# Optimization experiments

Measured on AMD Instinct MI355X. Metric: run time of the kernel, lower is better.

Reference implementation:

```python
import jax, jax.numpy as jnp
import numpy as np

N_CLASSES = 80
SEG_LEN = 512          # boxes per class (uniform segments)
H = 128                # hidden_size
DH = 2 * H             # decoder hidden (= concat of bidirectional encoder final hiddens)
EMB = 32               # decoder_input_dim
SOS, EOS = 2, 3


def _gru_cell(x, h, Wih, Whh, bih, bhh):
    # PyTorch GRU cell math. x:(in,), h:(hid,), Wih:(3*hid,in), Whh:(3*hid,hid)
    gi = Wih @ x + bih
    gh = Whh @ h + bhh
    i_r, i_z, i_n = jnp.split(gi, 3)
    h_r, h_z, h_n = jnp.split(gh, 3)
    r = jax.nn.sigmoid(i_r + h_r)
    z = jax.nn.sigmoid(i_z + h_z)
    n = jnp.tanh(i_n + r * h_n)
    return (1.0 - z) * n + z * h


def _gru_seq(xs, h0, Wih, Whh, bih, bhh):
    # xs: (T, in); returns final hidden (hid,) and all hiddens (T, hid)
    def step(h, x):
        h2 = _gru_cell(x, h, Wih, Whh, bih, bhh)
        return h2, h2
    hT, hs = jax.lax.scan(step, h0, xs)
    return hT, hs

# vmap over the 80 classes (per-class weights)
_run_gru = jax.vmap(_gru_seq, in_axes=(0, 0, 0, 0, 0, 0))


def setup_inputs() -> dict:
    key = jax.random.key(0)
    ks = jax.random.split(key, 32)
    N = N_CLASSES * SEG_LEN
    s = 0.05
    inp = {
        "feat": jax.random.normal(ks[0], (N, 1024), jnp.float32),
        "score": jax.random.uniform(ks[1], (N, 1), jnp.float32),
        "box": jax.random.uniform(ks[2], (N, 4), jnp.float32),
        "origin_score": jax.random.uniform(ks[3], (N, 91), jnp.float32),
        "labels": jax.random.randint(ks[4], (N,), 0, 2, jnp.int64),
        "weights": jax.random.uniform(ks[5], (N,), jnp.float32),
        "unique_class": jnp.ones((N_CLASSES,), jnp.int64),
        "unique_class_len": jnp.arange(N_CLASSES + 1, dtype=jnp.int64) * SEG_LEN,
        # shared linears
        "appear_W": jax.random.normal(ks[6], (H, 1024), jnp.float32) * s,
        "appear_b": jnp.zeros((H,), jnp.float32),
        "featlin_W": jax.random.normal(ks[7], (H, H + 96), jnp.float32) * s,
        "featlin_b": jnp.zeros((H,), jnp.float32),
        # per-class bidirectional encoder GRUs
        "enc_Wih_f": jax.random.normal(ks[8], (N_CLASSES, 3 * H, H), jnp.float32) * s,
        "enc_Whh_f": jax.random.normal(ks[9], (N_CLASSES, 3 * H, H), jnp.float32) * s,
        "enc_bih_f": jnp.zeros((N_CLASSES, 3 * H), jnp.float32),
        "enc_bhh_f": jnp.zeros((N_CLASSES, 3 * H), jnp.float32),
        "enc_Wih_b": jax.random.normal(ks[10], (N_CLASSES, 3 * H, H), jnp.float32) * s,
        "enc_Whh_b": jax.random.normal(ks[11], (N_CLASSES, 3 * H, H), jnp.float32) * s,
        "enc_bih_b": jnp.zeros((N_CLASSES, 3 * H), jnp.float32),
        "enc_bhh_b": jnp.zeros((N_CLASSES, 3 * H), jnp.float32),
        # decoder
        "dec_emb": jax.random.normal(ks[12], (4, EMB), jnp.float32) * s,
        "dec_Wih": jax.random.normal(ks[13], (N_CLASSES, 3 * DH, EMB), jnp.float32) * s,
        "dec_Whh": jax.random.normal(ks[14], (N_CLASSES, 3 * DH, DH), jnp.float32) * s,
        "dec_bih": jnp.zeros((N_CLASSES, 3 * DH), jnp.float32),
        "dec_bhh": jnp.zeros((N_CLASSES, 3 * DH), jnp.float32),
        "out_W": jax.random.normal(ks[15], (4, DH), jnp.float32) * s,
        "out_b": jnp.zeros((4,), jnp.float32),
    }
    return inp


def reference(feat, score, box, origin_score, labels, weights, unique_class,
              unique_class_len, appear_W, appear_b, featlin_W, featlin_b,
              enc_Wih_f, enc_Whh_f, enc_bih_f, enc_bhh_f,
              enc_Wih_b, enc_Whh_b, enc_bih_b, enc_bhh_b,
              dec_emb, dec_Wih, dec_Whh, dec_bih, dec_bhh, out_W, out_b):
    # --- shared feature encoding ---
    x = jax.nn.relu(feat @ appear_W.T + appear_b)                    # (N, H)
    allf = jnp.concatenate([x, score, box, origin_score], axis=1)    # (N, H+96)
    enc_feat = jax.nn.relu(allf @ featlin_W.T + featlin_b)           # (N, H)

    # --- per-class bidirectional encoder (uniform segments) ---
    seg = enc_feat.reshape(N_CLASSES, SEG_LEN, H)
    eos = jnp.ones((N_CLASSES, 1, H), enc_feat.dtype)                # encoder_EOS = ones
    enc_in = jnp.concatenate([seg, eos], axis=1)                     # (80, L+1, H)
    h0 = jnp.zeros((N_CLASSES, H), enc_feat.dtype)
    h_f, _ = _run_gru(enc_in, h0, enc_Wih_f, enc_Whh_f, enc_bih_f, enc_bhh_f)
    h_b, _ = _run_gru(enc_in[:, ::-1], h0, enc_Wih_b, enc_Whh_b, enc_bih_b, enc_bhh_b)
    dec_h0 = jnp.concatenate([h_f, h_b], axis=-1)                    # (80, 2H)

    # --- per-class decoder with teacher forcing (SOS then gold labels) ---
    emb = dec_emb[labels].reshape(N_CLASSES, SEG_LEN, EMB)
    sos = jnp.broadcast_to(dec_emb[SOS], (N_CLASSES, 1, EMB))
    dec_in = jnp.concatenate([sos, emb], axis=1)                     # (80, L+1, EMB)
    _, dec_hs = _run_gru(dec_in, dec_h0, dec_Wih, dec_Whh, dec_bih, dec_bhh)

    logits = dec_hs.reshape(-1, DH) @ out_W.T + out_b                # (80*(L+1), 4)
    output = jax.nn.log_softmax(logits, axis=-1)
    return output, labels, weights
```

## Files before the change

kernel.cpp:

```cpp
#include <hip/hip_runtime.h>


typedef __fp16 h2v __attribute__((ext_vector_type(2)));
typedef __fp16 h8 __attribute__((ext_vector_type(8)));

__device__ __forceinline__ h2v pk2(float a, float b) {
  return __builtin_amdgcn_cvt_pkrtz(a, b);
}
__device__ __forceinline__ unsigned h2u(h2v h) { return __builtin_bit_cast(unsigned, h); }
__device__ __forceinline__ h2v u2h(unsigned u) { return __builtin_bit_cast(h2v, u); }
__device__ __forceinline__ float fdot2f(h2v a, h2v b, float c) {
  return __builtin_amdgcn_fdot2(a, b, c, false);
}
__device__ __forceinline__ float sigf(float x) { return 1.f / (1.f + __expf(-x)); }
__device__ __forceinline__ float tanhfast(float x) { return 2.f / (1.f + __expf(-2.f * x)) - 1.f; }

__device__ __forceinline__ h8 pack8(float4 a, float4 b) {
  h2v p0 = pk2(a.x, a.y), p1 = pk2(a.z, a.w), p2 = pk2(b.x, b.y), p3 = pk2(b.z, b.w);
  return (h8){p0[0], p0[1], p1[0], p1[1], p2[0], p2[1], p3[0], p3[1]};
}

#define SL(V, j) (__builtin_shufflevector((V), (V), 2 * (j), 2 * (j) + 1))

template <int CTRL>
__device__ __forceinline__ float dppadd(float acc, float v) {
  int r = __builtin_amdgcn_update_dpp(0, __float_as_int(v), CTRL, 0xF, 0xF, true);
  return acc + __int_as_float(r);
}
__device__ __forceinline__ float swz4add(float acc, float v) {
  return acc + __int_as_float(__builtin_amdgcn_ds_swizzle(__float_as_int(v), 0x101F));
}

__device__ __forceinline__ float reduce8s(float p0, float p1, float p2, float p3,
                                          float p4, float p5, float p6, float p7) {
  p0 = dppadd<0xB1>(p0, p1);
  p2 = dppadd<0xB1>(p2, p3);
  p4 = dppadd<0xB1>(p4, p5);
  p6 = dppadd<0xB1>(p6, p7);
  p0 = dppadd<0x4E>(p0, p2);
  p4 = dppadd<0x4E>(p4, p6);
  p0 = swz4add(p0, p4);
  p0 = dppadd<0x128>(p0, p0);
  return p0;
}

__device__ __forceinline__ float dot4(h8 V, h2v a0, h2v a1, h2v a2, h2v a3, float acc) {
  acc = fdot2f(SL(V, 0), a0, acc);
  acc = fdot2f(SL(V, 1), a1, acc);
  acc = fdot2f(SL(V, 2), a2, acc);
  acc = fdot2f(SL(V, 3), a3, acc);
  return acc;
}

__global__ void k_fill_misc(const float* __restrict__ score, const float* __restrict__ box,
                            const float* __restrict__ orig, float* __restrict__ allf) {
  int i = blockIdx.x * blockDim.x + threadIdx.x;
  if (i >= 40960 * 96) return;
  int row = i / 96, k = i - row * 96;
  float v;
  if (k == 0) v = score[row];
  else if (k < 5) v = box[row * 4 + (k - 1)];
  else v = orig[(size_t)row * 91 + (k - 5)];
  allf[(size_t)row * 224 + 128 + k] = v;
}

__global__ __launch_bounds__(256) void k_gemm_appear(
    const float* __restrict__ A, const float* __restrict__ W,
    const float* __restrict__ bias, float* __restrict__ allf) {
  __shared__ float As[32][68];
  __shared__ float Ws[32][132];
  const int tid = threadIdx.x;
  const int tx = tid & 15, ty = tid >> 4;
  const int r0 = blockIdx.x * 64;
  const int lr = tid >> 3;
  const int lk = (tid & 7) * 4;
  float acc[4][8];
#pragma unroll
  for (int i = 0; i < 4; ++i)
#pragma unroll
    for (int j = 0; j < 8; ++j) acc[i][j] = 0.f;

  for (int k0 = 0; k0 < 1024; k0 += 32) {
#pragma unroll
    for (int i = 0; i < 2; ++i) {
      int rr = lr + i * 32;
      float4 v = *(const float4*)(A + (size_t)(r0 + rr) * 1024 + k0 + lk);
      As[lk + 0][rr] = v.x; As[lk + 1][rr] = v.y; As[lk + 2][rr] = v.z; As[lk + 3][rr] = v.w;
    }
#pragma unroll
    for (int i = 0; i < 4; ++i) {
      int wr = lr + i * 32;
      float4 v = *(const float4*)(W + (size_t)wr * 1024 + k0 + lk);
      Ws[lk + 0][wr] = v.x; Ws[lk + 1][wr] = v.y; Ws[lk + 2][wr] = v.z; Ws[lk + 3][wr] = v.w;
    }
    __syncthreads();
#pragma unroll
    for (int kk = 0; kk < 32; ++kk) {
      float4 a = *(const float4*)&As[kk][ty * 4];
      float4 w0 = *(const float4*)&Ws[kk][tx * 8];
      float4 w1 = *(const float4*)&Ws[kk][tx * 8 + 4];
      float av[4] = {a.x, a.y, a.z, a.w};
      float wv[8] = {w0.x, w0.y, w0.z, w0.w, w1.x, w1.y, w1.z, w1.w};
#pragma unroll
      for (int i = 0; i < 4; ++i)
#pragma unroll
        for (int j = 0; j < 8; ++j) acc[i][j] = fmaf(av[i], wv[j], acc[i][j]);
    }
    __syncthreads();
  }
#pragma unroll
  for (int i = 0; i < 4; ++i) {
    int row = r0 + ty * 4 + i;
#pragma unroll
    for (int j = 0; j < 8; ++j) {
      int col = tx * 8 + j;
      float v = acc[i][j] + bias[col];
      allf[(size_t)row * 224 + col] = fmaxf(v, 0.f);
    }
  }
}

__global__ __launch_bounds__(256) void k_gemm_featlin(
    const float* __restrict__ A, const float* __restrict__ W,
    const float* __restrict__ bias, unsigned* __restrict__ encf2) {
  __shared__ float As[32][68];
  __shared__ float Ws[32][132];
  const int tid = threadIdx.x;
  const int tx = tid & 15, ty = tid >> 4;
  const int r0 = blockIdx.x * 64;
  const int lr = tid >> 3;
  const int lk = (tid & 7) * 4;
  float acc[4][8];
#pragma unroll
  for (int i = 0; i < 4; ++i)
#pragma unroll
    for (int j = 0; j < 8; ++j) acc[i][j] = 0.f;

  for (int k0 = 0; k0 < 224; k0 += 32) {
#pragma unroll
    for (int i = 0; i < 2; ++i) {
      int rr = lr + i * 32;
      float4 v = *(const float4*)(A + (size_t)(r0 + rr) * 224 + k0 + lk);
      As[lk + 0][rr] = v.x; As[lk + 1][rr] = v.y; As[lk + 2][rr] = v.z; As[lk + 3][rr] = v.w;
    }
#pragma unroll
    for (int i = 0; i < 4; ++i) {
      int wr = lr + i * 32;
      float4 v = *(const float4*)(W + (size_t)wr * 224 + k0 + lk);
      Ws[lk + 0][wr] = v.x; Ws[lk + 1][wr] = v.y; Ws[lk + 2][wr] = v.z; Ws[lk + 3][wr] = v.w;
    }
    __syncthreads();
#pragma unroll
    for (int kk = 0; kk < 32; ++kk) {
      float4 a = *(const float4*)&As[kk][ty * 4];
      float4 w0 = *(const float4*)&Ws[kk][tx * 8];
      float4 w1 = *(const float4*)&Ws[kk][tx * 8 + 4];
      float av[4] = {a.x, a.y, a.z, a.w};
      float wv[8] = {w0.x, w0.y, w0.z, w0.w, w1.x, w1.y, w1.z, w1.w};
#pragma unroll
      for (int i = 0; i < 4; ++i)
#pragma unroll
        for (int j = 0; j < 8; ++j) acc[i][j] = fmaf(av[i], wv[j], acc[i][j]);
    }
    __syncthreads();
  }
#pragma unroll
  for (int i = 0; i < 4; ++i) {
    int row = r0 + ty * 4 + i;
    unsigned* orow = encf2 + (size_t)row * 64;
#pragma unroll
    for (int p = 0; p < 4; ++p) {
      int col = tx * 8 + 2 * p;
      float a = fmaxf(acc[i][2 * p] + bias[col], 0.f);
      float b = fmaxf(acc[i][2 * p + 1] + bias[col + 1], 0.f);
      orow[tx * 4 + p] = h2u(pk2(a, b));
    }
  }
}

__global__ __launch_bounds__(256) void k_dec_gi(
    const float* __restrict__ Wih, const float* __restrict__ bih,
    const float* __restrict__ emb, float* __restrict__ gi) {
  __shared__ float e[4][32];
  const int c = blockIdx.x, tid = threadIdx.x;
  if (tid < 128) e[tid >> 5][tid & 31] = emb[tid];
  __syncthreads();
#pragma unroll
  for (int i = 0; i < 3; ++i) {
    int r = tid + i * 256;
    const float* w = Wih + ((size_t)c * 768 + r) * 32;
    float b = bih[(size_t)c * 768 + r];
    float a0 = b, a1 = b, a2 = b, a3 = b;
#pragma unroll
    for (int k = 0; k < 32; ++k) {
      float wv = w[k];
      a0 = fmaf(wv, e[0][k], a0);
      a1 = fmaf(wv, e[1][k], a1);
      a2 = fmaf(wv, e[2][k], a2);
      a3 = fmaf(wv, e[3][k], a3);
    }
    gi[((size_t)c * 4 + 0) * 768 + r] = a0;
    gi[((size_t)c * 4 + 1) * 768 + r] = a1;
    gi[((size_t)c * 4 + 2) * 768 + r] = a2;
    gi[((size_t)c * 4 + 3) * 768 + r] = a3;
  }
}

#define ENCROW(k)                                                                   \
  h8 ci_##k, ch_##k, sg_##k;                                                        \
  {                                                                                 \
    int vc = 32 * w + 8 * q + ((k) ^ mw);                                           \
    const float4* pi = (const float4*)(Wih + (size_t)vc * 128 + 8 * m);             \
    ci_##k = pack8(pi[0], pi[1]);                                                   \
    __builtin_amdgcn_sched_barrier(0);                                              \
    const float4* ph = (const float4*)(Whh + (size_t)vc * 128 + 8 * m);             \
    ch_##k = pack8(ph[0], ph[1]);                                                   \
    __builtin_amdgcn_sched_barrier(0);                                              \
    int s = (w < 4) ? vc : (vc - 128);                                              \
    const float* sb =                                                               \
        (w < 4) ? (Wih + (size_t)(256 + s) * 128) : (Whh + (size_t)(256 + s) * 128);\
    const float4* ps = (const float4*)(sb + 8 * m);                                 \
    sg_##k = pack8(ps[0], ps[1]);                                                   \
    __builtin_amdgcn_sched_barrier(0);                                              \
  }

#define EDOTC(k) dot4(ci_##k, x0, x1, x2, x3, dot4(ch_##k, g0, g1, g2, g3, 0.f))
#define EDOTS(k) dot4(sg_##k, s0, s1, s2, s3, 0.f)

__global__ __launch_bounds__(512)
__attribute__((amdgpu_waves_per_eu(2, 2))) void k_enc_gru(
    const unsigned* __restrict__ encf2,
    const float* __restrict__ WihF, const float* __restrict__ WhhF,
    const float* __restrict__ bihF, const float* __restrict__ bhhF,
    const float* __restrict__ WihB, const float* __restrict__ WhhB,
    const float* __restrict__ bihB, const float* __restrict__ bhhB,
    float* __restrict__ dec_h0) {
  const int blk = blockIdx.x;
  const int c = blk >> 1, dir = blk & 1;
  const int tid = threadIdx.x;
  const int w = tid >> 6, l = tid & 63, q = l >> 4, m = l & 15, mw = m & 7;

  const float* Wih = (dir ? WihB : WihF) + (size_t)c * 384 * 128;
  const float* Whh = (dir ? WhhB : WhhF) + (size_t)c * 384 * 128;
  const float* bih = (dir ? bihB : bihF) + (size_t)c * 384;
  const float* bhh = (dir ? bhhB : bhhF) + (size_t)c * 384;

  __shared__ __align__(16) unsigned x2s[2][64];
  __shared__ __align__(16) unsigned h2s[64];
  __shared__ float aBuf[512];

  ENCROW(0) ENCROW(1) ENCROW(2) ENCROW(3)
  ENCROW(4) ENCROW(5) ENCROW(6) ENCROW(7)

  float bown;
  int ownIdx;
  if (m < 8) {
    int vo = 32 * w + 8 * q + m;
    bown = bih[vo] + bhh[vo];
    ownIdx = vo;
  } else {
    int so = (w < 4) ? (32 * w + 8 * q + mw) : (32 * (w - 4) + 8 * q + mw);
    bown = (w < 4) ? bih[256 + so] : bhh[256 + so];
    ownIdx = (w < 4) ? (256 + so) : (384 + so);
  }

  if (tid < 64) h2s[tid] = 0u;
  if (tid >= 448) {
    int lane = tid - 448;
    x2s[0][lane] = (dir == 0) ? encf2[((size_t)c * 512 + 0) * 64 + lane] : 0x3C003C00u;
  }
  float hreg = 0.f;
  __syncthreads();

  for (int t = 0; t <= 512; ++t) {
    unsigned xpre = 0;
    if (tid >= 448 && t < 512) {
      int tn = t + 1, lane = tid - 448;
      int row = (dir == 0) ? ((tn < 512) ? tn : -1) : (512 - tn);
      xpre = (row < 0) ? 0x3C003C00u : encf2[((size_t)c * 512 + row) * 64 + lane];
    }
    uint4 xv = ((const uint4*)&x2s[t & 1][0])[m];
    uint4 hv = ((const uint4*)&h2s[0])[m];
    h2v x0 = u2h(xv.x), x1 = u2h(xv.y), x2 = u2h(xv.z), x3 = u2h(xv.w);
    h2v g0 = u2h(hv.x), g1 = u2h(hv.y), g2 = u2h(hv.z), g3 = u2h(hv.w);
    float pA = reduce8s(EDOTC(0), EDOTC(1), EDOTC(2), EDOTC(3),
                        EDOTC(4), EDOTC(5), EDOTC(6), EDOTC(7));
    h2v s0 = (w < 4) ? x0 : g0, s1 = (w < 4) ? x1 : g1;
    h2v s2 = (w < 4) ? x2 : g2, s3 = (w < 4) ? x3 : g3;
    float pB = reduce8s(EDOTS(0), EDOTS(1), EDOTS(2), EDOTS(3),
                        EDOTS(4), EDOTS(5), EDOTS(6), EDOTS(7));
    aBuf[ownIdx] = ((m < 8) ? pA : pB) + bown;
    __syncthreads();
    if (tid < 128) {
      float r = sigf(aBuf[tid]);
      float z = sigf(aBuf[128 + tid]);
      float nn = tanhfast(aBuf[256 + tid] + r * aBuf[384 + tid]);
      float hn = (1.f - z) * nn + z * hreg;
      hreg = hn;
      float other = __shfl_xor(hn, 1, 64);
      if ((tid & 1) == 0) h2s[tid >> 1] = h2u(pk2(hn, other));
    } else if (tid >= 448 && t < 512) {
      x2s[(t + 1) & 1][tid - 448] = xpre;
    }
    __syncthreads();
  }
  if (tid < 128) dec_h0[(size_t)c * 256 + dir * 128 + tid] = hreg;
}

#define DECROW(kc, k)                                                               \
  h8 wA##kc##_##k, wB##kc##_##k;                                                    \
  {                                                                                 \
    int row = 64 * w + 16 * q + 8 * (kc) + ((k) ^ mw);                              \
    const float4* src = (const float4*)(Whh + ((size_t)c * 768 + row) * 256 + 16 * m);\
    float4 v0 = src[0], v1 = src[1];                                                \
    wA##kc##_##k = pack8(v0, v1);                                                   \
    __builtin_amdgcn_sched_barrier(0);                                              \
    float4 v2 = src[2], v3 = src[3];                                                \
    wB##kc##_##k = pack8(v2, v3);                                                   \
    __builtin_amdgcn_sched_barrier(0);                                              \
  }

#define DDOT(kc, k)                                                        \
  (fdot2f(SL(wB##kc##_##k, 3), g7,                                         \
   fdot2f(SL(wB##kc##_##k, 2), g6,                                         \
   fdot2f(SL(wB##kc##_##k, 1), g5,                                         \
   fdot2f(SL(wB##kc##_##k, 0), g4,                                         \
   fdot2f(SL(wA##kc##_##k, 3), g3,                                         \
   fdot2f(SL(wA##kc##_##k, 2), g2,                                         \
   fdot2f(SL(wA##kc##_##k, 1), g1,                                         \
   fdot2f(SL(wA##kc##_##k, 0), g0, 0.f)))))))))

__global__ __launch_bounds__(768)
__attribute__((amdgpu_waves_per_eu(3, 3))) void k_dec_gru(
    const float* __restrict__ Whh, const float* __restrict__ bhh,
    const float* __restrict__ gi, const float* __restrict__ h0,
    const int* __restrict__ labels,
    const float* __restrict__ outW, const float* __restrict__ outB,
    float* __restrict__ out) {
  const int c = blockIdx.x, tid = threadIdx.x;
  const int w = tid >> 6, l = tid & 63, q = l >> 4, m = l & 15, mw = m & 7;

  __shared__ __align__(16) unsigned h2s[128];
  __shared__ float aBuf[768];
  __shared__ float gisf[2304];
  __shared__ float owsh[1024];
  __shared__ int labs[513];
  __shared__ float red[4][4];

  DECROW(0, 0) DECROW(0, 1) DECROW(0, 2) DECROW(0, 3)
  DECROW(0, 4) DECROW(0, 5) DECROW(0, 6) DECROW(0, 7)
  DECROW(1, 0) DECROW(1, 1) DECROW(1, 2) DECROW(1, 3)
  DECROW(1, 4) DECROW(1, 5) DECROW(1, 6) DECROW(1, 7)

  float bown = bhh[(size_t)c * 768 + 64 * w + l];

  for (int i = tid; i < 2304; i += 768) gisf[i] = gi[(size_t)c * 4 * 768 + i];
  for (int i = tid; i < 1024; i += 768) owsh[i] = outW[i];
  if (tid < 512) labs[tid + 1] = labels[(size_t)c * 512 + tid];
  if (tid == 512) labs[0] = 2;
  float b0 = outB[0], b1 = outB[1], b2 = outB[2], b3 = outB[3];
  float hreg = 0.f;
  if (tid < 256) {
    hreg = h0[(size_t)c * 256 + tid];
    float other = __shfl_xor(hreg, 1, 64);
    if ((tid & 1) == 0) h2s[tid >> 1] = h2u(pk2(hreg, other));
  }
  __syncthreads();

  for (int t = 0; t <= 512; ++t) {
    const uint4* hp = (const uint4*)(&h2s[0]);
    uint4 ha = hp[2 * m], hb = hp[2 * m + 1];
    h2v g0 = u2h(ha.x), g1 = u2h(ha.y), g2 = u2h(ha.z), g3 = u2h(ha.w);
    h2v g4 = u2h(hb.x), g5 = u2h(hb.y), g6 = u2h(hb.z), g7 = u2h(hb.w);
    float pc0 = reduce8s(DDOT(0, 0), DDOT(0, 1), DDOT(0, 2), DDOT(0, 3),
                         DDOT(0, 4), DDOT(0, 5), DDOT(0, 6), DDOT(0, 7));
    float pc1 = reduce8s(DDOT(1, 0), DDOT(1, 1), DDOT(1, 2), DDOT(1, 3),
                         DDOT(1, 4), DDOT(1, 5), DDOT(1, 6), DDOT(1, 7));
    aBuf[64 * w + l] = ((m < 8) ? pc0 : pc1) + bown;
    __syncthreads();
    if (tid < 256) {
      int sel = labs[t];
      const float* gsel = &gisf[sel * 768];
      float r = sigf(gsel[tid] + aBuf[tid]);
      float z = sigf(gsel[256 + tid] + aBuf[256 + tid]);
      float nn = tanhfast(gsel[512 + tid] + r * aBuf[512 + tid]);
      float hn = (1.f - z) * nn + z * hreg;
      hreg = hn;
      float other = __shfl_xor(hn, 1, 64);
      if ((tid & 1) == 0) h2s[tid >> 1] = h2u(pk2(hn, other));
      float p0 = owsh[tid] * hn, p1 = owsh[256 + tid] * hn;
      float p2 = owsh[512 + tid] * hn, p3 = owsh[768 + tid] * hn;
#pragma unroll
      for (int off = 32; off > 0; off >>= 1) {
        p0 += __shfl_xor(p0, off, 64);
        p1 += __shfl_xor(p1, off, 64);
        p2 += __shfl_xor(p2, off, 64);
        p3 += __shfl_xor(p3, off, 64);
      }
      if ((tid & 63) == 0) {
        int ww = tid >> 6;
        red[ww][0] = p0; red[ww][1] = p1; red[ww][2] = p2; red[ww][3] = p3;
      }
    }
    __syncthreads();
    if (tid == 0) {
      float l0 = red[0][0] + red[1][0] + red[2][0] + red[3][0] + b0;
      float l1 = red[0][1] + red[1][1] + red[2][1] + red[3][1] + b1;
      float l2 = red[0][2] + red[1][2] + red[2][2] + red[3][2] + b2;
      float l3 = red[0][3] + red[1][3] + red[2][3] + red[3][3] + b3;
      float mm = fmaxf(fmaxf(l0, l1), fmaxf(l2, l3));
      float s = __expf(l0 - mm) + __expf(l1 - mm) + __expf(l2 - mm) + __expf(l3 - mm);
      float lse = mm + __logf(s);
      float* o = out + ((size_t)c * 513 + t) * 4;
      o[0] = l0 - lse; o[1] = l1 - lse; o[2] = l2 - lse; o[3] = l3 - lse;
    }
  }
}

__global__ void k_passthrough(const int* __restrict__ labels,
                              const float* __restrict__ weights,
                              float* __restrict__ out) {
  int i = blockIdx.x * blockDim.x + threadIdx.x;
  if (i < 40960) {
    out[164160 + i] = (float)labels[i];
    out[164160 + 40960 + i] = weights[i];
  }
}

extern "C" void kernel_launch(void* const* d_in, const int* in_sizes, int n_in,
                              void* d_out, int out_size, void* d_ws, size_t ws_size,
                              hipStream_t stream) {
  (void)in_sizes; (void)n_in; (void)out_size; (void)ws_size;
  const float* feat = (const float*)d_in[0];
  const float* score = (const float*)d_in[1];
  const float* box = (const float*)d_in[2];
  const float* orig = (const float*)d_in[3];
  const int* labels = (const int*)d_in[4];
  const float* weights = (const float*)d_in[5];
  const float* appear_W = (const float*)d_in[8];
  const float* appear_b = (const float*)d_in[9];
  const float* featlin_W = (const float*)d_in[10];
  const float* featlin_b = (const float*)d_in[11];
  const float* eWihF = (const float*)d_in[12];
  const float* eWhhF = (const float*)d_in[13];
  const float* ebihF = (const float*)d_in[14];
  const float* ebhhF = (const float*)d_in[15];
  const float* eWihB = (const float*)d_in[16];
  const float* eWhhB = (const float*)d_in[17];
  const float* ebihB = (const float*)d_in[18];
  const float* ebhhB = (const float*)d_in[19];
  const float* dec_emb = (const float*)d_in[20];
  const float* dWih = (const float*)d_in[21];
  const float* dWhh = (const float*)d_in[22];
  const float* dbih = (const float*)d_in[23];
  const float* dbhh = (const float*)d_in[24];
  const float* outW = (const float*)d_in[25];
  const float* outB = (const float*)d_in[26];
  float* out = (float*)d_out;

  char* ws = (char*)d_ws;
  float* allf = (float*)ws;
  unsigned* encf2 = (unsigned*)(ws + (size_t)40960 * 224 * 4);
  float* dec_h0 = (float*)(ws + (size_t)40960 * 224 * 4 + (size_t)40960 * 64 * 4);
  float* dec_gi = dec_h0 + 80 * 256;

  k_fill_misc<<<15360, 256, 0, stream>>>(score, box, orig, allf);
  k_gemm_appear<<<640, 256, 0, stream>>>(feat, appear_W, appear_b, allf);
  k_gemm_featlin<<<640, 256, 0, stream>>>(allf, featlin_W, featlin_b, encf2);
  k_dec_gi<<<80, 256, 0, stream>>>(dWih, dbih, dec_emb, dec_gi);
  k_enc_gru<<<160, 512, 0, stream>>>(encf2, eWihF, eWhhF, ebihF, ebhhF,
                                     eWihB, eWhhB, ebihB, ebhhB, dec_h0);
  k_dec_gru<<<80, 768, 0, stream>>>(dWhh, dbhh, dec_gi, dec_h0, labels, outW, outB, out);
  k_passthrough<<<160, 256, 0, stream>>>(labels, weights, out);
}
```

Baseline: 1.653 ms.

## Restructure encoder/decoder GRU steps to one barrier per step, split output projection

Both recurrent kernels are reorganised so each thread computes a full hidden unit's gates, with partners combined via lane shuffles. This removes the shared-memory gate buffer and cuts each timestep to a single barrier using double-buffered hidden state. Decoder weights are pre-packed to fp16 in a separate kernel, split across registers, LDS and per-step global streaming, and the block shrinks to 512 threads. The output projection and log-softmax move out of the serial loop into a parallel kernel over stored fp16 hidden states, at the cost of extra launches and workspace traffic.

After: 1.595 ms. 3.5% less time.

```diff
diff --git a/kernel.cpp b/kernel.cpp
--- a/kernel.cpp
+++ b/kernel.cpp
@@ -2,7 +2,6 @@
 
 
 typedef __fp16 h2v __attribute__((ext_vector_type(2)));
-typedef __fp16 h8 __attribute__((ext_vector_type(8)));
 
 __device__ __forceinline__ h2v pk2(float a, float b) {
   return __builtin_amdgcn_cvt_pkrtz(a, b);
@@ -15,12 +14,21 @@
 __device__ __forceinline__ float sigf(float x) { return 1.f / (1.f + __expf(-x)); }
 __device__ __forceinline__ float tanhfast(float x) { return 2.f / (1.f + __expf(-2.f * x)) - 1.f; }
 
-__device__ __forceinline__ h8 pack8(float4 a, float4 b) {
-  h2v p0 = pk2(a.x, a.y), p1 = pk2(a.z, a.w), p2 = pk2(b.x, b.y), p3 = pk2(b.z, b.w);
-  return (h8){p0[0], p0[1], p1[0], p1[1], p2[0], p2[1], p3[0], p3[1]};
-}
-
-#define SL(V, j) (__builtin_shufflevector((V), (V), 2 * (j), 2 * (j) + 1))
+__device__ __forceinline__ uint4 pack8u(float4 a, float4 b) {
+  uint4 o;
+  o.x = h2u(pk2(a.x, a.y)); o.y = h2u(pk2(a.z, a.w));
+  o.z = h2u(pk2(b.x, b.y)); o.w = h2u(pk2(b.z, b.w));
+  return o;
+}
+
+__device__ __forceinline__ float dotu4(uint4 cv, h2v a0, h2v a1, h2v a2, h2v a3,
+                                       float acc) {
+  acc = fdot2f(u2h(cv.x), a0, acc);
+  acc = fdot2f(u2h(cv.y), a1, acc);
+  acc = fdot2f(u2h(cv.z), a2, acc);
+  acc = fdot2f(u2h(cv.w), a3, acc);
+  return acc;
+}
 
 template <int CTRL>
 __device__ __forceinline__ float dppadd(float acc, float v) {
@@ -44,13 +52,10 @@
   return p0;
 }
 
-__device__ __forceinline__ float dot4(h8 V, h2v a0, h2v a1, h2v a2, h2v a3, float acc) {
-  acc = fdot2f(SL(V, 0), a0, acc);
-  acc = fdot2f(SL(V, 1), a1, acc);
-  acc = fdot2f(SL(V, 2), a2, acc);
-  acc = fdot2f(SL(V, 3), a3, acc);
-  return acc;
-}
+#define BAR_LGKM()                                     \
+  asm volatile("s_waitcnt lgkmcnt(0)" ::: "memory");   \
+  __builtin_amdgcn_s_barrier();                        \
+  asm volatile("" ::: "memory");
 
 __global__ void k_fill_misc(const float* __restrict__ score, const float* __restrict__ box,
                             const float* __restrict__ orig, float* __restrict__ allf) {
@@ -206,29 +211,30 @@
   }
 }
 
-#define ENCROW(k)                                                                   \
-  h8 ci_##k, ch_##k, sg_##k;                                                        \
-  {                                                                                 \
-    int vc = 32 * w + 8 * q + ((k) ^ mw);                                           \
-    const float4* pi = (const float4*)(Wih + (size_t)vc * 128 + 8 * m);             \
-    ci_##k = pack8(pi[0], pi[1]);                                                   \
-    __builtin_amdgcn_sched_barrier(0);                                              \
-    const float4* ph = (const float4*)(Whh + (size_t)vc * 128 + 8 * m);             \
-    ch_##k = pack8(ph[0], ph[1]);                                                   \
-    __builtin_amdgcn_sched_barrier(0);                                              \
-    int s = (w < 4) ? vc : (vc - 128);                                              \
-    const float* sb =                                                               \
-        (w < 4) ? (Wih + (size_t)(256 + s) * 128) : (Whh + (size_t)(256 + s) * 128);\
-    const float4* ps = (const float4*)(sb + 8 * m);                                 \
-    sg_##k = pack8(ps[0], ps[1]);                                                   \
-    __builtin_amdgcn_sched_barrier(0);                                              \
-  }
-
-#define EDOTC(k) dot4(ci_##k, x0, x1, x2, x3, dot4(ch_##k, g0, g1, g2, g3, 0.f))
-#define EDOTS(k) dot4(sg_##k, s0, s1, s2, s3, 0.f)
-
-__global__ __launch_bounds__(512)
-__attribute__((amdgpu_waves_per_eu(2, 2))) void k_enc_gru(
+__global__ __launch_bounds__(512) void k_pack_dec(
+    const float* __restrict__ Whh, uint4* __restrict__ wpk) {
+  const int c = blockIdx.x / 48, ic = blockIdx.x % 48;
+  const int tid = threadIdx.x;
+  const int G = tid >> 4, m = tid & 15, mw = m & 7;
+  const int gt = ic >> 4, k = (ic & 15) >> 1, hf = ic & 1;
+  const int row = gt * 256 + 8 * G + (k ^ mw);
+  const float* src = Whh + ((size_t)c * 768 + row) * 256 + 16 * m + 8 * hf;
+  wpk[((size_t)c * 48 + ic) * 512 + tid] =
+      pack8u(*(const float4*)src, *(const float4*)(src + 4));
+}
+
+#define ELOAD(gt, k, DST)                                                          \
+  {                                                                                \
+    int rid_ = (k) ^ mw;                                                           \
+    const float* Mx_ = ((k) & 1) ? baseB : baseA;                                  \
+    const float4* ps_ =                                                            \
+        (const float4*)(Mx_ + ((size_t)((gt) * 128 + 4 * G + (rid_ >> 1))) * 128 + \
+                        8 * m);                                                    \
+    DST = pack8u(ps_[0], ps_[1]);                                                  \
+  }                                                                                \
+  __builtin_amdgcn_sched_barrier(0);
+
+__global__ __launch_bounds__(512) void k_enc_gru(
     const unsigned* __restrict__ encf2,
     const float* __restrict__ WihF, const float* __restrict__ WhhF,
     const float* __restrict__ bihF, const float* __restrict__ bhhF,
@@ -238,39 +244,55 @@
   const int blk = blockIdx.x;
   const int c = blk >> 1, dir = blk & 1;
   const int tid = threadIdx.x;
-  const int w = tid >> 6, l = tid & 63, q = l >> 4, m = l & 15, mw = m & 7;
+  const int G = tid >> 4, m = tid & 15, mw = m & 7;
 
   const float* Wih = (dir ? WihB : WihF) + (size_t)c * 384 * 128;
   const float* Whh = (dir ? WhhB : WhhF) + (size_t)c * 384 * 128;
   const float* bih = (dir ? bihB : bihF) + (size_t)c * 384;
   const float* bhh = (dir ? bhhB : bhhF) + (size_t)c * 384;
 
+  const float* baseA = (mw & 1) ? Whh : Wih;
+  const float* baseB = (mw & 1) ? Wih : Whh;
+
   __shared__ __align__(16) unsigned x2s[2][64];
-  __shared__ __align__(16) unsigned h2s[64];
-  __shared__ float aBuf[512];
-
-  ENCROW(0) ENCROW(1) ENCROW(2) ENCROW(3)
-  ENCROW(4) ENCROW(5) ENCROW(6) ENCROW(7)
-
-  float bown;
-  int ownIdx;
-  if (m < 8) {
-    int vo = 32 * w + 8 * q + m;
-    bown = bih[vo] + bhh[vo];
-    ownIdx = vo;
-  } else {
-    int so = (w < 4) ? (32 * w + 8 * q + mw) : (32 * (w - 4) + 8 * q + mw);
-    bown = (w < 4) ? bih[256 + so] : bhh[256 + so];
-    ownIdx = (w < 4) ? (256 + so) : (384 + so);
-  }
-
-  if (tid < 64) h2s[tid] = 0u;
+  __shared__ __align__(16) unsigned h2s[2][64];
+  __shared__ __align__(16) uint4 wle[12 * 512];
+
+  uint4 er0, er1, er2, er3, er4, er5, er6, er7, ez0, ez1, ez2, ez3;
+  ELOAD(0, 0, er0) ELOAD(0, 1, er1) ELOAD(0, 2, er2) ELOAD(0, 3, er3)
+  ELOAD(0, 4, er4) ELOAD(0, 5, er5) ELOAD(0, 6, er6) ELOAD(0, 7, er7)
+  ELOAD(1, 0, ez0) ELOAD(1, 1, ez1) ELOAD(1, 2, ez2) ELOAD(1, 3, ez3)
+  {
+    uint4 t0;
+    ELOAD(1, 4, t0) wle[0 * 512 + tid] = t0;
+    ELOAD(1, 5, t0) wle[1 * 512 + tid] = t0;
+    ELOAD(1, 6, t0) wle[2 * 512 + tid] = t0;
+    ELOAD(1, 7, t0) wle[3 * 512 + tid] = t0;
+    ELOAD(2, 0, t0) wle[4 * 512 + tid] = t0;
+    ELOAD(2, 1, t0) wle[5 * 512 + tid] = t0;
+    ELOAD(2, 2, t0) wle[6 * 512 + tid] = t0;
+    ELOAD(2, 3, t0) wle[7 * 512 + tid] = t0;
+    ELOAD(2, 4, t0) wle[8 * 512 + tid] = t0;
+    ELOAD(2, 5, t0) wle[9 * 512 + tid] = t0;
+    ELOAD(2, 6, t0) wle[10 * 512 + tid] = t0;
+    ELOAD(2, 7, t0) wle[11 * 512 + tid] = t0;
+  }
+
+  const int u = 4 * G + (mw >> 1);
+  const float brz_r = bih[u] + bhh[u];
+  const float brz_z = bih[128 + u] + bhh[128 + u];
+  const float b_in = bih[256 + u];
+  const float b_hn = bhh[256 + u];
+
+  if (tid < 64) h2s[0][tid] = 0u;
   if (tid >= 448) {
     int lane = tid - 448;
     x2s[0][lane] = (dir == 0) ? encf2[((size_t)c * 512 + 0) * 64 + lane] : 0x3C003C00u;
   }
   float hreg = 0.f;
   __syncthreads();
+
+  const uint4* wl = wle + tid;
 
   for (int t = 0; t <= 512; ++t) {
     unsigned xpre = 0;
@@ -280,140 +302,167 @@
       xpre = (row < 0) ? 0x3C003C00u : encf2[((size_t)c * 512 + row) * 64 + lane];
     }
     uint4 xv = ((const uint4*)&x2s[t & 1][0])[m];
-    uint4 hv = ((const uint4*)&h2s[0])[m];
+    uint4 hv = ((const uint4*)&h2s[t & 1][0])[m];
     h2v x0 = u2h(xv.x), x1 = u2h(xv.y), x2 = u2h(xv.z), x3 = u2h(xv.w);
-    h2v g0 = u2h(hv.x), g1 = u2h(hv.y), g2 = u2h(hv.z), g3 = u2h(hv.w);
-    float pA = reduce8s(EDOTC(0), EDOTC(1), EDOTC(2), EDOTC(3),
-                        EDOTC(4), EDOTC(5), EDOTC(6), EDOTC(7));
-    h2v s0 = (w < 4) ? x0 : g0, s1 = (w < 4) ? x1 : g1;
-    h2v s2 = (w < 4) ? x2 : g2, s3 = (w < 4) ? x3 : g3;
-    float pB = reduce8s(EDOTS(0), EDOTS(1), EDOTS(2), EDOTS(3),
-                        EDOTS(4), EDOTS(5), EDOTS(6), EDOTS(7));
-    aBuf[ownIdx] = ((m < 8) ? pA : pB) + bown;
-    __syncthreads();
-    if (tid < 128) {
-      float r = sigf(aBuf[tid]);
-      float z = sigf(aBuf[128 + tid]);
-      float nn = tanhfast(aBuf[256 + tid] + r * aBuf[384 + tid]);
-      float hn = (1.f - z) * nn + z * hreg;
-      hreg = hn;
-      float other = __shfl_xor(hn, 1, 64);
-      if ((tid & 1) == 0) h2s[tid >> 1] = h2u(pk2(hn, other));
-    } else if (tid >= 448 && t < 512) {
-      x2s[(t + 1) & 1][tid - 448] = xpre;
-    }
-    __syncthreads();
-  }
-  if (tid < 128) dec_h0[(size_t)c * 256 + dir * 128 + tid] = hreg;
-}
-
-#define DECROW(kc, k)                                                               \
-  h8 wA##kc##_##k, wB##kc##_##k;                                                    \
-  {                                                                                 \
-    int row = 64 * w + 16 * q + 8 * (kc) + ((k) ^ mw);                              \
-    const float4* src = (const float4*)(Whh + ((size_t)c * 768 + row) * 256 + 16 * m);\
-    float4 v0 = src[0], v1 = src[1];                                                \
-    wA##kc##_##k = pack8(v0, v1);                                                   \
-    __builtin_amdgcn_sched_barrier(0);                                              \
-    float4 v2 = src[2], v3 = src[3];                                                \
-    wB##kc##_##k = pack8(v2, v3);                                                   \
-    __builtin_amdgcn_sched_barrier(0);                                              \
-  }
-
-#define DDOT(kc, k)                                                        \
-  (fdot2f(SL(wB##kc##_##k, 3), g7,                                         \
-   fdot2f(SL(wB##kc##_##k, 2), g6,                                         \
-   fdot2f(SL(wB##kc##_##k, 1), g5,                                         \
-   fdot2f(SL(wB##kc##_##k, 0), g4,                                         \
-   fdot2f(SL(wA##kc##_##k, 3), g3,                                         \
-   fdot2f(SL(wA##kc##_##k, 2), g2,                                         \
-   fdot2f(SL(wA##kc##_##k, 1), g1,                                         \
-   fdot2f(SL(wA##kc##_##k, 0), g0, 0.f)))))))))
-
-__global__ __launch_bounds__(768)
-__attribute__((amdgpu_waves_per_eu(3, 3))) void k_dec_gru(
-    const float* __restrict__ Whh, const float* __restrict__ bhh,
+    h2v hh0 = u2h(hv.x), hh1 = u2h(hv.y), hh2 = u2h(hv.z), hh3 = u2h(hv.w);
+    bool oddl = (mw & 1);
+    h2v a0 = oddl ? hh0 : x0, a1 = oddl ? hh1 : x1, a2 = oddl ? hh2 : x2, a3 = oddl ? hh3 : x3;
+    h2v b0 = oddl ? x0 : hh0, b1 = oddl ? x1 : hh1, b2 = oddl ? x2 : hh2, b3 = oddl ? x3 : hh3;
+#define EA(ch) dotu4(ch, a0, a1, a2, a3, 0.f)
+#define EB(ch) dotu4(ch, b0, b1, b2, b3, 0.f)
+    float vR = reduce8s(EA(er0), EB(er1), EA(er2), EB(er3),
+                        EA(er4), EB(er5), EA(er6), EB(er7));
+    float vZ = reduce8s(EA(ez0), EB(ez1), EA(ez2), EB(ez3),
+                        EA(wl[0 * 512]), EB(wl[1 * 512]), EA(wl[2 * 512]), EB(wl[3 * 512]));
+    float vN = reduce8s(EA(wl[4 * 512]), EB(wl[5 * 512]), EA(wl[6 * 512]), EB(wl[7 * 512]),
+                        EA(wl[8 * 512]), EB(wl[9 * 512]), EA(wl[10 * 512]), EB(wl[11 * 512]));
+#undef EA
+#undef EB
+    float oR = __shfl_xor(vR, 1, 64);
+    float oZ = __shfl_xor(vZ, 1, 64);
+    float oN = __shfl_xor(vN, 1, 64);
+    float r = sigf(vR + oR + brz_r);
+    float z = sigf(vZ + oZ + brz_z);
+    float i_n = oddl ? oN : vN;
+    float h_n = oddl ? vN : oN;
+    float n = tanhfast(i_n + b_in + r * (h_n + b_hn));
+    float hn = (1.f - z) * n + z * hreg;
+    hreg = hn;
+    float prt = __shfl_xor(hn, 2, 64);
+    if (m < 8 && (mw & 3) == 0) h2s[(t + 1) & 1][2 * G + (mw >> 2)] = h2u(pk2(hn, prt));
+    if (tid >= 448 && t < 512) x2s[(t + 1) & 1][tid - 448] = xpre;
+    BAR_LGKM();
+  }
+  if ((m < 8) && ((mw & 1) == 0))
+    dec_h0[(size_t)c * 256 + dir * 128 + u] = hreg;
+}
+
+#define CONSX(sa, sb) dotu4(sb, g4, g5, g6, g7, dotu4(sa, g0, g1, g2, g3, 0.f))
+
+__global__ __launch_bounds__(512) void k_dec_gru(
+    const uint4* __restrict__ wpk, const float* __restrict__ bhh,
     const float* __restrict__ gi, const float* __restrict__ h0,
-    const int* __restrict__ labels,
-    const float* __restrict__ outW, const float* __restrict__ outB,
-    float* __restrict__ out) {
+    const int* __restrict__ labels, unsigned* __restrict__ dhs2) {
   const int c = blockIdx.x, tid = threadIdx.x;
-  const int w = tid >> 6, l = tid & 63, q = l >> 4, m = l & 15, mw = m & 7;
-
-  __shared__ __align__(16) unsigned h2s[128];
-  __shared__ float aBuf[768];
-  __shared__ float gisf[2304];
-  __shared__ float owsh[1024];
+  const int G = tid >> 4, m = tid & 15, mw = m & 7;
+
+  __shared__ __align__(16) unsigned h2s[2][128];
   __shared__ int labs[513];
-  __shared__ float red[4][4];
-
-  DECROW(0, 0) DECROW(0, 1) DECROW(0, 2) DECROW(0, 3)
-  DECROW(0, 4) DECROW(0, 5) DECROW(0, 6) DECROW(0, 7)
-  DECROW(1, 0) DECROW(1, 1) DECROW(1, 2) DECROW(1, 3)
-  DECROW(1, 4) DECROW(1, 5) DECROW(1, 6) DECROW(1, 7)
-
-  float bown = bhh[(size_t)c * 768 + 64 * w + l];
-
-  for (int i = tid; i < 2304; i += 768) gisf[i] = gi[(size_t)c * 4 * 768 + i];
-  for (int i = tid; i < 1024; i += 768) owsh[i] = outW[i];
+  __shared__ __align__(16) uint4 wlds[19 * 512];
+
+  const uint4* wp = wpk + (size_t)c * 48 * 512 + tid;
+  const uint4* wpS = wp + 31 * 512;
+
+  for (int j = 0; j < 19; ++j) wlds[j * 512 + tid] = wp[(12 + j) * 512];
+  __builtin_amdgcn_sched_barrier(0);
+  uint4 ua0 = wp[0 * 512], ua1 = wp[1 * 512], ua2 = wp[2 * 512], ua3 = wp[3 * 512];
+  uint4 ua4 = wp[4 * 512], ua5 = wp[5 * 512], ua6 = wp[6 * 512], ua7 = wp[7 * 512];
+  uint4 ua8 = wp[8 * 512], ua9 = wp[9 * 512], ua10 = wp[10 * 512], ua11 = wp[11 * 512];
+  __builtin_amdgcn_sched_barrier(0);
+  uint4 sl0 = wpS[0 * 512], sl1 = wpS[1 * 512], sl2 = wpS[2 * 512], sl3 = wpS[3 * 512];
+  uint4 sl4 = wpS[4 * 512], sl5 = wpS[5 * 512], sl6 = wpS[6 * 512], sl7 = wpS[7 * 512];
+
+  const int u = 8 * G + mw;
+  const float bb0 = bhh[(size_t)c * 768 + u];
+  const float bb1 = bhh[(size_t)c * 768 + 256 + u];
+  const float bb2 = bhh[(size_t)c * 768 + 512 + u];
+  const float* gib = gi + (size_t)c * 4 * 768;
+  unsigned* dout = dhs2 + (size_t)c * 513 * 128 + 4 * G + (mw >> 1);
+
   if (tid < 512) labs[tid + 1] = labels[(size_t)c * 512 + tid];
-  if (tid == 512) labs[0] = 2;
-  float b0 = outB[0], b1 = outB[1], b2 = outB[2], b3 = outB[3];
-  float hreg = 0.f;
-  if (tid < 256) {
-    hreg = h0[(size_t)c * 256 + tid];
-    float other = __shfl_xor(hreg, 1, 64);
-    if ((tid & 1) == 0) h2s[tid >> 1] = h2u(pk2(hreg, other));
+  if (tid == 0) labs[0] = 2;
+  float hreg = h0[(size_t)c * 256 + u];
+  {
+    float oth = __shfl_xor(hreg, 1, 64);
+    if (m < 8 && (mw & 1) == 0) h2s[0][4 * G + (mw >> 1)] = h2u(pk2(hreg, oth));
   }
   __syncthreads();
 
+  const uint4* wl = wlds + tid;
+
   for (int t = 0; t <= 512; ++t) {
-    const uint4* hp = (const uint4*)(&h2s[0]);
-    uint4 ha = hp[2 * m], hb = hp[2 * m + 1];
+    uint4 ha = ((const uint4*)&h2s[t & 1][0])[2 * m];
+    uint4 hb = ((const uint4*)&h2s[t & 1][0])[2 * m + 1];
     h2v g0 = u2h(ha.x), g1 = u2h(ha.y), g2 = u2h(ha.z), g3 = u2h(ha.w);
     h2v g4 = u2h(hb.x), g5 = u2h(hb.y), g6 = u2h(hb.z), g7 = u2h(hb.w);
-    float pc0 = reduce8s(DDOT(0, 0), DDOT(0, 1), DDOT(0, 2), DDOT(0, 3),
-                         DDOT(0, 4), DDOT(0, 5), DDOT(0, 6), DDOT(0, 7));
-    float pc1 = reduce8s(DDOT(1, 0), DDOT(1, 1), DDOT(1, 2), DDOT(1, 3),
-                         DDOT(1, 4), DDOT(1, 5), DDOT(1, 6), DDOT(1, 7));
-    aBuf[64 * w + l] = ((m < 8) ? pc0 : pc1) + bown;
-    __syncthreads();
-    if (tid < 256) {
-      int sel = labs[t];
-      const float* gsel = &gisf[sel * 768];
-      float r = sigf(gsel[tid] + aBuf[tid]);
-      float z = sigf(gsel[256 + tid] + aBuf[256 + tid]);
-      float nn = tanhfast(gsel[512 + tid] + r * aBuf[512 + tid]);
-      float hn = (1.f - z) * nn + z * hreg;
-      hreg = hn;
-      float other = __shfl_xor(hn, 1, 64);
-      if ((tid & 1) == 0) h2s[tid >> 1] = h2u(pk2(hn, other));
-      float p0 = owsh[tid] * hn, p1 = owsh[256 + tid] * hn;
-      float p2 = owsh[512 + tid] * hn, p3 = owsh[768 + tid] * hn;
-#pragma unroll
-      for (int off = 32; off > 0; off >>= 1) {
-        p0 += __shfl_xor(p0, off, 64);
-        p1 += __shfl_xor(p1, off, 64);
-        p2 += __shfl_xor(p2, off, 64);
-        p3 += __shfl_xor(p3, off, 64);
-      }
-      if ((tid & 63) == 0) {
-        int ww = tid >> 6;
-        red[ww][0] = p0; red[ww][1] = p1; red[ww][2] = p2; red[ww][3] = p3;
-      }
-    }
-    __syncthreads();
-    if (tid == 0) {
-      float l0 = red[0][0] + red[1][0] + red[2][0] + red[3][0] + b0;
-      float l1 = red[0][1] + red[1][1] + red[2][1] + red[3][1] + b1;
-      float l2 = red[0][2] + red[1][2] + red[2][2] + red[3][2] + b2;
-      float l3 = red[0][3] + red[1][3] + red[2][3] + red[3][3] + b3;
-      float mm = fmaxf(fmaxf(l0, l1), fmaxf(l2, l3));
-      float s = __expf(l0 - mm) + __expf(l1 - mm) + __expf(l2 - mm) + __expf(l3 - mm);
-      float lse = mm + __logf(s);
-      float* o = out + ((size_t)c * 513 + t) * 4;
-      o[0] = l0 - lse; o[1] = l1 - lse; o[2] = l2 - lse; o[3] = l3 - lse;
-    }
+    int sel = labs[t];
+    const float* gp = gib + sel * 768;
+    float giR = gp[u], giZ = gp[256 + u], giN = gp[512 + u];
+    uint4 dj = wp[47 * 512];
+    float p0 = CONSX(ua0, ua1), p1 = CONSX(ua2, ua3);
+    float p2 = CONSX(ua4, ua5), p3 = CONSX(ua6, ua7);
+    float p4 = CONSX(ua8, ua9), p5 = CONSX(ua10, ua11);
+    float p6 = CONSX(wl[0 * 512], wl[1 * 512]);
+    float p7 = CONSX(wl[2 * 512], wl[3 * 512]);
+    float rsum = reduce8s(p0, p1, p2, p3, p4, p5, p6, p7);
+    p0 = CONSX(wl[4 * 512], wl[5 * 512]);
+    p1 = CONSX(wl[6 * 512], wl[7 * 512]);
+    p2 = CONSX(wl[8 * 512], wl[9 * 512]);
+    p3 = CONSX(wl[10 * 512], wl[11 * 512]);
+    p4 = CONSX(wl[12 * 512], wl[13 * 512]);
+    p5 = CONSX(wl[14 * 512], wl[15 * 512]);
+    p6 = CONSX(wl[16 * 512], wl[17 * 512]);
+    p7 = CONSX(wl[18 * 512], sl0);
+    sl0 = wpS[8 * 512];
+    float zsum = reduce8s(p0, p1, p2, p3, p4, p5, p6, p7);
+    p0 = CONSX(sl1, sl2); sl1 = wpS[9 * 512]; sl2 = wpS[10 * 512];
+    p1 = CONSX(sl3, sl4); sl3 = wpS[11 * 512]; sl4 = wpS[12 * 512];
+    p2 = CONSX(sl5, sl6); sl5 = wpS[13 * 512]; sl6 = wpS[14 * 512];
+    p3 = CONSX(sl7, sl0); sl7 = wpS[15 * 512]; sl0 = wpS[0 * 512];
+    p4 = CONSX(sl1, sl2); sl1 = wpS[1 * 512]; sl2 = wpS[2 * 512];
+    p5 = CONSX(sl3, sl4); sl3 = wpS[3 * 512]; sl4 = wpS[4 * 512];
+    p6 = CONSX(sl5, sl6); sl5 = wpS[5 * 512]; sl6 = wpS[6 * 512];
+    p7 = CONSX(sl7, dj);  sl7 = wpS[7 * 512];
+    float nsum = reduce8s(p0, p1, p2, p3, p4, p5, p6, p7);
+    float r = sigf(giR + rsum + bb0);
+    float z = sigf(giZ + zsum + bb1);
+    float n = tanhfast(giN + r * (nsum + bb2));
+    float hn = (1.f - z) * n + z * hreg;
+    hreg = hn;
+    float oth = __shfl_xor(hn, 1, 64);
+    if (m < 8 && (mw & 1) == 0) {
+      unsigned pk = h2u(pk2(hn, oth));
+      h2s[(t + 1) & 1][4 * G + (mw >> 1)] = pk;
+      dout[(size_t)t * 128] = pk;
+    }
+    BAR_LGKM();
+  }
+}
+
+__global__ __launch_bounds__(256) void k_out(
+    const unsigned* __restrict__ dhs2, const float* __restrict__ outW,
+    const float* __restrict__ outB, float* __restrict__ out) {
+  int row = blockIdx.x * 4 + (threadIdx.x >> 6);
+  if (row >= 41040) return;
+  int lane = threadIdx.x & 63;
+  const unsigned* hp = dhs2 + (size_t)row * 128 + 2 * lane;
+  h2v ha = u2h(hp[0]), hb = u2h(hp[1]);
+  float h0f = (float)ha[0], h1f = (float)ha[1], h2f = (float)hb[0], h3f = (float)hb[1];
+  float p0, p1, p2, p3;
+  {
+    const float* w0 = outW + 4 * lane;
+    const float* w1 = outW + 256 + 4 * lane;
+    const float* w2 = outW + 512 + 4 * lane;
+    const float* w3 = outW + 768 + 4 * lane;
+    p0 = h0f * w0[0] + h1f * w0[1] + h2f * w0[2] + h3f * w0[3];
+    p1 = h0f * w1[0] + h1f * w1[1] + h2f * w1[2] + h3f * w1[3];
+    p2 = h0f * w2[0] + h1f * w2[1] + h2f * w2[2] + h3f * w2[3];
+    p3 = h0f * w3[0] + h1f * w3[1] + h2f * w3[2] + h3f * w3[3];
+  }
+#pragma unroll
+  for (int off = 32; off > 0; off >>= 1) {
+    p0 += __shfl_xor(p0, off, 64);
+    p1 += __shfl_xor(p1, off, 64);
+    p2 += __shfl_xor(p2, off, 64);
+    p3 += __shfl_xor(p3, off, 64);
+  }
+  if (lane == 0) {
+    float l0 = p0 + outB[0], l1 = p1 + outB[1], l2 = p2 + outB[2], l3 = p3 + outB[3];
+    float mm = fmaxf(fmaxf(l0, l1), fmaxf(l2, l3));
+    float s = __expf(l0 - mm) + __expf(l1 - mm) + __expf(l2 - mm) + __expf(l3 - mm);
+    float lse = mm + __logf(s);
+    float* o = out + (size_t)row * 4;
+    o[0] = l0 - lse; o[1] = l1 - lse; o[2] = l2 - lse; o[3] = l3 - lse;
   }
 }
 
@@ -463,13 +512,17 @@
   unsigned* encf2 = (unsigned*)(ws + (size_t)40960 * 224 * 4);
   float* dec_h0 = (float*)(ws + (size_t)40960 * 224 * 4 + (size_t)40960 * 64 * 4);
   float* dec_gi = dec_h0 + 80 * 256;
+  unsigned* dhs2 = (unsigned*)(dec_gi + 80 * 4 * 768);
+  uint4* wpack = (uint4*)allf;
 
   k_fill_misc<<<15360, 256, 0, stream>>>(score, box, orig, allf);
   k_gemm_appear<<<640, 256, 0, stream>>>(feat, appear_W, appear_b, allf);
   k_gemm_featlin<<<640, 256, 0, stream>>>(allf, featlin_W, featlin_b, encf2);
+  k_pack_dec<<<80 * 48, 512, 0, stream>>>(dWhh, wpack);
   k_dec_gi<<<80, 256, 0, stream>>>(dWih, dbih, dec_emb, dec_gi);
   k_enc_gru<<<160, 512, 0, stream>>>(encf2, eWihF, eWhhF, ebihF, ebhhF,
                                      eWihB, eWhhB, ebihB, ebhhB, dec_h0);
-  k_dec_gru<<<80, 768, 0, stream>>>(dWhh, dbhh, dec_gi, dec_h0, labels, outW, outB, out);
+  k_dec_gru<<<80, 512, 0, stream>>>(wpack, dbhh, dec_gi, dec_h0, labels, dhs2);
+  k_out<<<10260, 256, 0, stream>>>(dhs2, outW, outB, out);
   k_passthrough<<<160, 256, 0, stream>>>(labels, weights, out);
 }
```
